# Optimization experiments

Hardware: AMD Instinct MI355X
Metric: run time of the kernel (lower is better)

The kernel has to match this reference:

```python
import jax, jax.numpy as jnp
import numpy as np

B, LQ, LK = 8, 2048, 2048
HIST_DIM, COMB_DIM, FUSION_DIM = 1024, 1024, 1024


def _linear_params(key, in_dim, out_dim):
    k1, k2 = jax.random.split(key)
    bound = 1.0 / np.sqrt(in_dim)
    W = jax.random.uniform(k1, (out_dim, in_dim), jnp.float32, -bound, bound)
    b = jax.random.uniform(k2, (out_dim,), jnp.float32, -bound, bound)
    return W, b


def setup_inputs() -> dict:
    key = jax.random.key(0)
    ks = jax.random.split(key, 8)
    hW, hb = _linear_params(ks[0], HIST_DIM, FUSION_DIM)
    cW, cb = _linear_params(ks[1], COMB_DIM, FUSION_DIM)
    qW, qb = _linear_params(ks[2], FUSION_DIM, FUSION_DIM)
    kW, kb = _linear_params(ks[3], FUSION_DIM, FUSION_DIM)
    vW, vb = _linear_params(ks[4], FUSION_DIM, FUSION_DIM)
    oW, ob = _linear_params(ks[5], FUSION_DIM, FUSION_DIM)
    return {
        "history_features": jax.random.normal(ks[6], (B, LQ, HIST_DIM), jnp.float32),
        "combined_features": jax.random.normal(ks[7], (B, LK, COMB_DIM), jnp.float32),
        "hW": hW, "hb": hb, "cW": cW, "cb": cb,
        "qW": qW, "qb": qb, "kW": kW, "kb": kb,
        "vW": vW, "vb": vb, "oW": oW, "ob": ob,
    }


def _lin(x, W, b):
    # torch nn.Linear: y = x @ W.T + b
    return jnp.einsum('bld,fd->blf', x, W) + b


def reference(history_features, combined_features, hW, hb, cW, cb, qW, qb, kW, kb, vW, vb, oW, ob):
    h = _lin(history_features, hW, hb)      # [B, LQ, F]
    c = _lin(combined_features, cW, cb)     # [B, LK, F]
    q = _lin(h, qW, qb)
    k = _lin(c, kW, kb)
    v = _lin(c, vW, vb)
    scale = 1.0 / jnp.sqrt(jnp.float32(FUSION_DIM))
    scores = jnp.einsum('bqf,bkf->bqk', q, k) * scale
    attn = jax.nn.softmax(scores, axis=-1)
    attn_out = jnp.einsum('bqk,bkf->bqf', attn, v)
    return _lin(attn_out + q, oW, ob)
```

## Files before the change

kernel.cpp:

```cpp
#include <hip/hip_runtime.h>
#include <stdint.h>

using bf16x8 = __attribute__((ext_vector_type(8))) short;
using f32x4  = __attribute__((ext_vector_type(4))) float;
using u16x4  = __attribute__((ext_vector_type(4))) unsigned short;
using u16x8  = __attribute__((ext_vector_type(8))) unsigned short;

__device__ __forceinline__ unsigned short f2bf(float f) {
  unsigned u = __builtin_bit_cast(unsigned, f);
  u = (u + 0x7FFFu + ((u >> 16) & 1u)) >> 16;
  return (unsigned short)u;
}
__device__ __forceinline__ float bf2f(unsigned short h) {
  unsigned u = ((unsigned)h) << 16;
  return __builtin_bit_cast(float, u);
}

__global__ __launch_bounds__(256) void cvt_f32_to_bf16(
    const float* __restrict__ in, unsigned short* __restrict__ out, long n8) {
  long i = (long)blockIdx.x * blockDim.x + threadIdx.x;
  const long stride = (long)gridDim.x * blockDim.x;
  for (; i < n8; i += stride) {
    float4 a = ((const float4*)in)[2 * i];
    float4 b = ((const float4*)in)[2 * i + 1];
    u16x8 o = { f2bf(a.x), f2bf(a.y), f2bf(a.z), f2bf(a.w),
                f2bf(b.x), f2bf(b.y), f2bf(b.z), f2bf(b.w) };
    ((u16x8*)out)[i] = o;
  }
}

__global__ __launch_bounds__(256) void transpose_cast(
    const float* __restrict__ in, unsigned short* __restrict__ out, int R, int C) {
  __shared__ unsigned short tile[64][68];
  const int c0 = blockIdx.x * 64, r0 = blockIdx.y * 64;
  const int t = threadIdx.x;
#pragma unroll
  for (int i = 0; i < 4; ++i) {
    int ch = t + i * 256;
    int r = ch >> 4, c4 = (ch & 15) * 4;
    float4 v = *(const float4*)&in[(size_t)(r0 + r) * C + c0 + c4];
    u16x4 o = { f2bf(v.x), f2bf(v.y), f2bf(v.z), f2bf(v.w) };
    *(u16x4*)&tile[r][c4] = o;
  }
  __syncthreads();
#pragma unroll
  for (int i = 0; i < 4; ++i) {
    int ch = t + i * 256;
    int r = ch >> 4, c4 = (ch & 15) * 4;
    u16x4 v;
#pragma unroll
    for (int j = 0; j < 4; ++j) v[j] = tile[c4 + j][r];
    *(u16x4*)&out[(size_t)(c0 + r) * R + r0 + c4] = v;
  }
}

__global__ __launch_bounds__(256) void bias_matvec(
    const float* __restrict__ W, const float* __restrict__ x,
    const float* __restrict__ b, float* __restrict__ out, int n) {
  const int row = blockIdx.x;
  const float* wr = W + (long)row * n;
  float s = 0.f;
  for (int j = threadIdx.x; j < n; j += 256) s += wr[j] * x[j];
#pragma unroll
  for (int o = 32; o; o >>= 1) s += __shfl_xor(s, o);
  __shared__ float red[4];
  if ((threadIdx.x & 63) == 0) red[threadIdx.x >> 6] = s;
  __syncthreads();
  if (threadIdx.x == 0) out[row] = red[0] + red[1] + red[2] + red[3] + b[row];
}

__global__ __launch_bounds__(256) void merge_invl(
    const float* __restrict__ Lpart, float* __restrict__ invL, long nrows) {
  long r = (long)blockIdx.x * 256 + threadIdx.x;
  if (r < nrows) {
    const float* p = Lpart + r * 8;
    float s = 0.f;
#pragma unroll
    for (int i = 0; i < 8; ++i) s += p[i];
    invL[r] = 1.f / s;
  }
}

template <int EPI>
__global__ __launch_bounds__(256, 4) void gemm_bt(
    const unsigned short* __restrict__ A, const unsigned short* __restrict__ B,
    void* __restrict__ C, const float* __restrict__ bias,
    int M, int N, int K, float scale) {
  __shared__ unsigned short lA[2][128][32];
  __shared__ unsigned short lB[2][128][32];
  const int t = threadIdx.x;
  const int gx = gridDim.x, gy = gridDim.y;
  int bid = blockIdx.x + gx * blockIdx.y;
  const int nwg = gx * gy;
  const int chunk = nwg >> 3;
  int lid = (bid & 7) * chunk + (bid >> 3);
  const int bn = lid % gx;
  const int bm = lid / gx;

  const unsigned short* Ab = A + (long)bm * 128 * K;
  const unsigned short* Bb = B + (long)bn * 128 * K;

  const int lane = t & 63;
  const int wv = t >> 6, wm = wv >> 1, wn = wv & 1;
  const int fr = lane & 15, kg = lane >> 4;
  const int srow  = t >> 2;
  const int scol  = (t & 3) * 8;
  const int wbyte = (t >> 6) * 1024;

  f32x4 acc[4][4] = {};
  const int NT = K >> 5;

  auto stage = [&](int buf, int kt) {
    const unsigned short* sa = Ab + kt * 32;
    const unsigned short* sb = Bb + kt * 32;
#pragma unroll
    for (int p = 0; p < 2; ++p) {
      const unsigned short* srcA = sa + (long)(p * 64 + srow) * K + scol;
      const unsigned short* srcB = sb + (long)(p * 64 + srow) * K + scol;
      char* dA = (char*)(&lA[buf][0][0]) + p * 4096 + wbyte;
      char* dB = (char*)(&lB[buf][0][0]) + p * 4096 + wbyte;
      __builtin_amdgcn_global_load_lds(
          (const __attribute__((address_space(1))) void*)srcA,
          (__attribute__((address_space(3))) void*)dA, 16, 0, 0);
      __builtin_amdgcn_global_load_lds(
          (const __attribute__((address_space(1))) void*)srcB,
          (__attribute__((address_space(3))) void*)dB, 16, 0, 0);
    }
  };

  stage(0, 0);
  for (int kt = 0; kt < NT; ++kt) {
    const int cur = kt & 1;
    __syncthreads();
    if (kt + 1 < NT) stage(cur ^ 1, kt + 1);
    bf16x8 av[4], bv[4];
#pragma unroll
    for (int m = 0; m < 4; ++m)
      av[m] = *(const bf16x8*)&lA[cur][wm * 64 + m * 16 + fr][kg * 8];
#pragma unroll
    for (int n = 0; n < 4; ++n)
      bv[n] = *(const bf16x8*)&lB[cur][wn * 64 + n * 16 + fr][kg * 8];
#pragma unroll
    for (int m = 0; m < 4; ++m)
#pragma unroll
      for (int n = 0; n < 4; ++n)
        acc[m][n] = __builtin_amdgcn_mfma_f32_16x16x32_bf16(av[m], bv[n], acc[m][n], 0, 0, 0);
  }

  const int row0 = bm * 128 + wm * 64 + kg * 4;
  const int col0 = bn * 128 + wn * 64 + fr;
#pragma unroll
  for (int m = 0; m < 4; ++m)
#pragma unroll
    for (int n = 0; n < 4; ++n) {
      const int col = col0 + n * 16;
#pragma unroll
      for (int r = 0; r < 4; ++r) {
        const int row = row0 + m * 16 + r;
        float v = acc[m][n][r];
        if constexpr (EPI == 1) v *= scale; else v += bias[col];
        ((unsigned short*)C)[(long)row * N + col] = f2bf(v);
      }
    }
}

template <int EPI>
__global__ __launch_bounds__(512, 2) void gemm256(
    const unsigned short* __restrict__ A, const unsigned short* __restrict__ B,
    void* __restrict__ C, const float* __restrict__ bias,
    const unsigned short* __restrict__ resid, float* __restrict__ aux,
    int N, int K, long sA, long sB, long sC, long sR, float scale) {
  __shared__ char lds[131072];
  const int t = threadIdx.x;
  const int lane = t & 63, wid = t >> 6;

  const int gx = gridDim.x, gy = gridDim.y;
  int bid = blockIdx.x + gx * (blockIdx.y + gy * blockIdx.z);
  const int nwg = gx * gy * (int)gridDim.z;
  const int chunk = nwg >> 3;
  int lid = (bid & 7) * chunk + (bid >> 3);
  const int bn = lid % gx; lid /= gx;
  const int bm = lid % gy;
  const int bz = lid / gy;

  const unsigned short* Ab = A + (long)bz * sA + (long)bm * 256 * K;
  const unsigned short* Bb = B + (long)bz * sB + (long)bn * 256 * K;

  const int colswz = ((lane & 3) * 8) ^ ((lane >> 5) * 16);
  const int r0s = (wid >> 1) * 16 + (lane >> 2);
  const int scol = (wid & 1) * 32 + colswz;

  const unsigned short* aPtr = Ab + (long)r0s * K + scol;
  const unsigned short* bPtr = Bb + (long)r0s * K + scol;
  const long off_s = (long)64 * K;
  const int  widB  = wid * 1024;

  auto issue = [&](const unsigned short* p, int h, int bufbyte) {
#pragma unroll
    for (int s = 0; s < 2; ++s) {
      const unsigned short* src = p + (h * 2 + s) * off_s;
      char* dst = lds + bufbyte + h * 16384 + s * 8192 + widB;
      __builtin_amdgcn_global_load_lds(
          (const __attribute__((address_space(1))) void*)src,
          (__attribute__((address_space(3))) void*)dst, 16, 0, 0);
    }
  };

  const int wm = wid >> 2, wn = wid & 3;
  const int fr = lane & 15, kg = lane >> 4;
  const int lanePart = (fr * 64 + kg * 16) ^ ((fr >> 3) << 5);

  f32x4 acc[8][4] = {};
  const int NT = K >> 6;
  const int NITER = NT >> 1;

  issue(aPtr, 0, 0);          issue(aPtr, 1, 0);
  issue(bPtr, 0, 65536);      issue(bPtr, 1, 65536);
  issue(bPtr + 64, 0, 98304); issue(bPtr + 64, 1, 98304);
  asm volatile("s_waitcnt vmcnt(4)" ::: "memory");
  __builtin_amdgcn_s_barrier();

  for (int it = 0; it < NITER; ++it) {
    const bool last = (it == NITER - 1);
#pragma unroll
    for (int hf = 0; hf < 2; ++hf) {
      const char* aB = lds + hf * 32768 + wm * 16384 + lanePart;
      const char* bB = lds + 65536 + hf * 32768 + wn * 8192 + lanePart;
      bf16x8 bv[4][2];
      bf16x8 av[2][2];
#pragma unroll
      for (int mp = 0; mp < 4; ++mp) {
        if (mp == 0) {
#pragma unroll
          for (int n = 0; n < 4; ++n)
#pragma unroll
            for (int kk = 0; kk < 2; ++kk)
              bv[n][kk] = *(const bf16x8*)(bB + n * 2048 + kk * 1024);
        }
#pragma unroll
        for (int ml = 0; ml < 2; ++ml)
#pragma unroll
          for (int kk = 0; kk < 2; ++kk)
            av[ml][kk] = *(const bf16x8*)(aB + (mp * 2 + ml) * 2048 + kk * 1024);
        if (hf == 0) {
          if (mp == 0) issue(aPtr + 64, 0, 32768);
          else if (mp == 1) { issue(aPtr + 64, 1, 32768); if (!last) issue(bPtr + 128, 0, 65536); }
          else if (mp == 2) { if (!last) issue(bPtr + 128, 1, 65536); }
          else {
            if (last) asm volatile("s_waitcnt vmcnt(0)" ::: "memory");
            else      asm volatile("s_waitcnt vmcnt(4)" ::: "memory");
          }
        } else if (!last) {
          if (mp == 0) issue(aPtr + 128, 0, 0);
          else if (mp == 1) { issue(aPtr + 128, 1, 0); issue(bPtr + 192, 0, 98304); }
          else if (mp == 2) issue(bPtr + 192, 1, 98304);
          else asm volatile("s_waitcnt vmcnt(4)" ::: "memory");
        }
        __builtin_amdgcn_s_barrier();
        asm volatile("s_waitcnt lgkmcnt(0)" ::: "memory");
        __builtin_amdgcn_sched_barrier(0);
        __builtin_amdgcn_s_setprio(1);
#pragma unroll
        for (int kk = 0; kk < 2; ++kk)
#pragma unroll
          for (int ml = 0; ml < 2; ++ml)
#pragma unroll
            for (int n = 0; n < 4; ++n)
              acc[mp * 2 + ml][n] = __builtin_amdgcn_mfma_f32_16x16x32_bf16(
                  av[ml][kk], bv[n][kk], acc[mp * 2 + ml][n], 0, 0, 0);
        __builtin_amdgcn_s_setprio(0);
        __builtin_amdgcn_s_barrier();
      }
    }
    aPtr += 128;
    bPtr += 128;
  }

  const int row0 = bm * 256 + wm * 128 + kg * 4;
  const int col0 = bn * 256 + wn * 64 + fr;
  const long cb = (long)bz * sC;

  if constexpr (EPI == 5) {
    float* lf = (float*)lds;
#pragma unroll
    for (int m = 0; m < 8; ++m) {
#pragma unroll
      for (int r = 0; r < 4; ++r) {
        const int row = row0 + m * 16 + r;
        float sv = 0.f;
#pragma unroll
        for (int n = 0; n < 4; ++n) {
          float e = exp2f(acc[m][n][r] * scale);
          unsigned short eb = f2bf(e);
          ((unsigned short*)C)[cb + (long)row * N + col0 + n * 16] = eb;
          sv += bf2f(eb);
        }
#pragma unroll
        for (int o = 1; o < 16; o <<= 1) sv += __shfl_xor(sv, o);
        if ((lane & 15) == 0)
          lf[wn * 256 + wm * 128 + m * 16 + kg * 4 + r] = sv;
      }
    }
    __syncthreads();
    if (t < 256) {
      float s4 = lf[t] + lf[256 + t] + lf[512 + t] + lf[768 + t];
      aux[((long)bz * 2048 + bm * 256 + t) * 8 + bn] = s4;
    }
    return;
  }

#pragma unroll
  for (int m = 0; m < 8; ++m)
#pragma unroll
    for (int n = 0; n < 4; ++n) {
      const int col = col0 + n * 16;
#pragma unroll
      for (int r = 0; r < 4; ++r) {
        const int row = row0 + m * 16 + r;
        float v = acc[m][n][r];
        if constexpr (EPI == 0) {
          v += bias[col];
          ((unsigned short*)C)[cb + (long)row * N + col] = f2bf(v);
        } else if constexpr (EPI == 1) {
          v *= scale;
          ((unsigned short*)C)[cb + (long)row * N + col] = f2bf(v);
        } else if constexpr (EPI == 3) {
          v += bias[col];
          ((float*)C)[cb + (long)row * N + col] = v;
        } else if constexpr (EPI == 4) {
          v += bias[row];
          ((unsigned short*)C)[cb + (long)row * N + col] = f2bf(v);
        } else {
          v = v * bias[(long)bz * 2048 + row] + bf2f(resid[(long)bz * sR + (long)row * N + col]);
          ((unsigned short*)C)[cb + (long)row * N + col] = f2bf(v);
        }
      }
    }
}

extern "C" void kernel_launch(void* const* d_in, const int* in_sizes, int n_in,
                              void* d_out, int out_size, void* d_ws, size_t ws_size,
                              hipStream_t stream) {
  (void)in_sizes; (void)n_in; (void)out_size; (void)ws_size;
  const float* hist = (const float*)d_in[0];
  const float* comb = (const float*)d_in[1];
  const float* hW = (const float*)d_in[2];  const float* hb = (const float*)d_in[3];
  const float* cW = (const float*)d_in[4];  const float* cb = (const float*)d_in[5];
  const float* qW = (const float*)d_in[6];  const float* qb = (const float*)d_in[7];
  const float* kW = (const float*)d_in[8];
  const float* vW = (const float*)d_in[10]; const float* vb = (const float*)d_in[11];
  const float* oW = (const float*)d_in[12]; const float* ob = (const float*)d_in[13];

  constexpr int  Bn = 8, L = 2048, F = 1024;
  constexpr long NE = (long)Bn * L * F;
  constexpr long WE = (long)F * F;

  char* ws = (char*)d_ws;
  size_t off = 0;
  unsigned short* oWb = (unsigned short*)(ws + off); off += WE * 2;
  unsigned short* Wq  = (unsigned short*)(ws + off); off += WE * 2;
  unsigned short* Wkv = (unsigned short*)(ws + off); off += 2 * WE * 2;
  unsigned short* Wk  = Wkv;
  unsigned short* Wv  = Wkv + WE;
  float* bq = (float*)(ws + off); off += F * 4;
  float* bv = (float*)(ws + off); off += F * 4;
  float* Lpart = (float*)(ws + off); off += (size_t)Bn * L * 8 * 4;
  float* invL  = (float*)(ws + off); off += (size_t)Bn * L * 4;
  unsigned short* A0 = (unsigned short*)(ws + off); off += NE * 2;
  unsigned short* A1 = (unsigned short*)(ws + off); off += NE * 2;
  unsigned short* A2 = (unsigned short*)(ws + off); off += NE * 2;
  unsigned short* A3 = (unsigned short*)(ws + off); off += NE * 2;
  unsigned short* S  = (unsigned short*)(ws + off); off += (size_t)Bn * L * L * 2;
  unsigned short* hWt = S;
  unsigned short* cWt = S + WE;
  unsigned short* qWb = S + 2 * WE;
  unsigned short* kvWb = S + 3 * WE;

  transpose_cast<<<dim3(16, 16, 1), 256, 0, stream>>>(hW, hWt, F, F);
  transpose_cast<<<dim3(16, 16, 1), 256, 0, stream>>>(cW, cWt, F, F);
  cvt_f32_to_bf16<<<512, 256, 0, stream>>>(qW, qWb, WE / 8);
  cvt_f32_to_bf16<<<512, 256, 0, stream>>>(kW, kvWb, WE / 8);
  cvt_f32_to_bf16<<<512, 256, 0, stream>>>(vW, kvWb + WE, WE / 8);
  cvt_f32_to_bf16<<<512, 256, 0, stream>>>(oW, oWb, WE / 8);
  cvt_f32_to_bf16<<<2048, 256, 0, stream>>>(hist, A0, NE / 8);
  cvt_f32_to_bf16<<<2048, 256, 0, stream>>>(comb, A1, NE / 8);

  bias_matvec<<<F, 256, 0, stream>>>(qW, hb, qb, bq, F);
  bias_matvec<<<F, 256, 0, stream>>>(vW, cb, vb, bv, F);

  gemm_bt<1><<<dim3(8, 8, 1), 256, 0, stream>>>(qWb, hWt, Wq, nullptr,
      1024, 1024, 1024, 1.0f);
  gemm_bt<1><<<dim3(8, 16, 1), 256, 0, stream>>>(kvWb, cWt, Wkv, nullptr,
      2048, 1024, 1024, 1.0f);

  const float S2 = 0.03125f * 1.44269504089f;

  gemm256<0><<<dim3(4, 64, 1), 512, 0, stream>>>(A0, Wq, A2, bq, nullptr, nullptr,
      1024, 1024, 0, 0, 0, 0, 0.f);
  gemm256<1><<<dim3(4, 64, 1), 512, 0, stream>>>(A1, Wk, A0, nullptr, nullptr, nullptr,
      1024, 1024, 0, 0, 0, 0, 1.0f);
  gemm256<4><<<dim3(8, 4, Bn), 512, 0, stream>>>(Wv, A1, A3, bv, nullptr, nullptr,
      2048, 1024, 0, (long)L * F, (long)F * L, 0, 0.f);
  gemm256<5><<<dim3(8, 8, Bn), 512, 0, stream>>>(A2, A0, S, nullptr, nullptr, Lpart,
      2048, 1024, (long)L * F, (long)L * F, (long)L * L, 0, S2);
  merge_invl<<<64, 256, 0, stream>>>(Lpart, invL, (long)Bn * L);
  gemm256<6><<<dim3(4, 8, Bn), 512, 0, stream>>>(S, A3, A1, invL, A2, nullptr,
      1024, 2048, (long)L * L, (long)F * L, (long)L * F, (long)L * F, 0.f);
  gemm256<3><<<dim3(4, 64, 1), 512, 0, stream>>>(A1, oWb, (float*)d_out, ob, nullptr, nullptr,
      1024, 1024, 0, 0, 0, 0, 0.f);
}
```

Measured before the change: 400.4 us.

## Double-buffer LDS-to-register fragment loads to overlap with MFMA compute

Fragments for the next MFMA sub-step are now loaded from LDS into a second register set while the current sub-step's MFMAs run, and the per-step barriers drop from two to one. The goal is to hide LDS read latency behind matrix math instead of stalling on lgkmcnt before every MFMA block. In exchange the A/B fragment register use roughly doubles, which can cut occupancy, and the reordered vmcnt waits and barriers around the buffer switch could expose a race on the shared LDS tiles.

```diff
diff --git a/kernel.cpp b/kernel.cpp
--- a/kernel.cpp
+++ b/kernel.cpp
@@ -189,7 +189,6 @@
   const int colswz = ((lane & 3) * 8) ^ ((lane >> 5) * 16);
   const int r0s = (wid >> 1) * 16 + (lane >> 2);
   const int scol = (wid & 1) * 32 + colswz;
-
   const unsigned short* aPtr = Ab + (long)r0s * K + scol;
   const unsigned short* bPtr = Bb + (long)r0s * K + scol;
   const long off_s = (long)64 * K;
@@ -209,8 +208,14 @@
   const int wm = wid >> 2, wn = wid & 3;
   const int fr = lane & 15, kg = lane >> 4;
   const int lanePart = (fr * 64 + kg * 16) ^ ((fr >> 3) << 5);
+  const char* aB0 = lds + 0      + wm * 16384 + lanePart;
+  const char* aB1 = lds + 32768  + wm * 16384 + lanePart;
+  const char* bB0 = lds + 65536  + wn * 8192  + lanePart;
+  const char* bB1 = lds + 98304  + wn * 8192  + lanePart;
 
   f32x4 acc[8][4] = {};
+  bf16x8 avA[2][2], avB[2][2];
+  bf16x8 bvA[4][2], bvB[4][2];
   const int NT = K >> 6;
   const int NITER = NT >> 1;
 
@@ -219,46 +224,66 @@
   issue(bPtr + 64, 0, 98304); issue(bPtr + 64, 1, 98304);
   asm volatile("s_waitcnt vmcnt(4)" ::: "memory");
   __builtin_amdgcn_s_barrier();
+#pragma unroll
+  for (int n = 0; n < 4; ++n)
+#pragma unroll
+    for (int kk = 0; kk < 2; ++kk)
+      bvA[n][kk] = *(const bf16x8*)(bB0 + n * 2048 + kk * 1024);
+#pragma unroll
+  for (int ml = 0; ml < 2; ++ml)
+#pragma unroll
+    for (int kk = 0; kk < 2; ++kk)
+      avA[ml][kk] = *(const bf16x8*)(aB0 + ml * 2048 + kk * 1024);
+  asm volatile("s_waitcnt lgkmcnt(0)" ::: "memory");
+  __builtin_amdgcn_sched_barrier(0);
 
   for (int it = 0; it < NITER; ++it) {
     const bool last = (it == NITER - 1);
 #pragma unroll
     for (int hf = 0; hf < 2; ++hf) {
-      const char* aB = lds + hf * 32768 + wm * 16384 + lanePart;
-      const char* bB = lds + 65536 + hf * 32768 + wn * 8192 + lanePart;
-      bf16x8 bv[4][2];
-      bf16x8 av[2][2];
+      const char* aB  = hf ? aB1 : aB0;
+      const char* aBn = hf ? aB0 : aB1;
+      const char* bBn = hf ? bB0 : bB1;
 #pragma unroll
       for (int mp = 0; mp < 4; ++mp) {
-        if (mp == 0) {
-#pragma unroll
-          for (int n = 0; n < 4; ++n)
-#pragma unroll
-            for (int kk = 0; kk < 2; ++kk)
-              bv[n][kk] = *(const bf16x8*)(bB + n * 2048 + kk * 1024);
-        }
-#pragma unroll
-        for (int ml = 0; ml < 2; ++ml)
-#pragma unroll
-          for (int kk = 0; kk < 2; ++kk)
-            av[ml][kk] = *(const bf16x8*)(aB + (mp * 2 + ml) * 2048 + kk * 1024);
+        const int P = hf * 4 + mp;
+        bf16x8 (&avCur)[2][2] = (P & 1) ? avB : avA;
+        bf16x8 (&avNxt)[2][2] = (P & 1) ? avA : avB;
+        bf16x8 (&bvCur)[4][2] = hf ? bvB : bvA;
+        bf16x8 (&bvNxt)[4][2] = hf ? bvA : bvB;
+        const bool endAll = last && hf == 1 && mp == 3;
+
         if (hf == 0) {
           if (mp == 0) issue(aPtr + 64, 0, 32768);
           else if (mp == 1) { issue(aPtr + 64, 1, 32768); if (!last) issue(bPtr + 128, 0, 65536); }
           else if (mp == 2) { if (!last) issue(bPtr + 128, 1, 65536); }
-          else {
-            if (last) asm volatile("s_waitcnt vmcnt(0)" ::: "memory");
-            else      asm volatile("s_waitcnt vmcnt(4)" ::: "memory");
-          }
         } else if (!last) {
           if (mp == 0) issue(aPtr + 128, 0, 0);
           else if (mp == 1) { issue(aPtr + 128, 1, 0); issue(bPtr + 192, 0, 98304); }
           else if (mp == 2) issue(bPtr + 192, 1, 98304);
-          else asm volatile("s_waitcnt vmcnt(4)" ::: "memory");
         }
-        __builtin_amdgcn_s_barrier();
-        asm volatile("s_waitcnt lgkmcnt(0)" ::: "memory");
-        __builtin_amdgcn_sched_barrier(0);
+
+        if (!endAll) {
+          if (mp < 3) {
+#pragma unroll
+            for (int ml = 0; ml < 2; ++ml)
+#pragma unroll
+              for (int kk = 0; kk < 2; ++kk)
+                avNxt[ml][kk] = *(const bf16x8*)(aB + ((mp + 1) * 2 + ml) * 2048 + kk * 1024);
+          } else {
+#pragma unroll
+            for (int n = 0; n < 4; ++n)
+#pragma unroll
+              for (int kk = 0; kk < 2; ++kk)
+                bvNxt[n][kk] = *(const bf16x8*)(bBn + n * 2048 + kk * 1024);
+#pragma unroll
+            for (int ml = 0; ml < 2; ++ml)
+#pragma unroll
+              for (int kk = 0; kk < 2; ++kk)
+                avNxt[ml][kk] = *(const bf16x8*)(aBn + ml * 2048 + kk * 1024);
+          }
+        }
+
         __builtin_amdgcn_s_setprio(1);
 #pragma unroll
         for (int kk = 0; kk < 2; ++kk)
@@ -267,8 +292,21 @@
 #pragma unroll
             for (int n = 0; n < 4; ++n)
               acc[mp * 2 + ml][n] = __builtin_amdgcn_mfma_f32_16x16x32_bf16(
-                  av[ml][kk], bv[n][kk], acc[mp * 2 + ml][n], 0, 0, 0);
+                  avCur[ml][kk], bvCur[n][kk], acc[mp * 2 + ml][n], 0, 0, 0);
         __builtin_amdgcn_s_setprio(0);
+
+        if (mp == 2) {
+          if (hf == 0) {
+            if (last) asm volatile("s_waitcnt vmcnt(0) lgkmcnt(0)" ::: "memory");
+            else      asm volatile("s_waitcnt vmcnt(4) lgkmcnt(0)" ::: "memory");
+          } else {
+            if (last) asm volatile("s_waitcnt lgkmcnt(0)" ::: "memory");
+            else      asm volatile("s_waitcnt vmcnt(4) lgkmcnt(0)" ::: "memory");
+          }
+        } else {
+          asm volatile("s_waitcnt lgkmcnt(0)" ::: "memory");
+        }
+        __builtin_amdgcn_sched_barrier(0);
         __builtin_amdgcn_s_barrier();
       }
     }
```

Measured after the change: 564.5 us. 1.41x slower.
